# Optimization experiments

Hardware: AMD Instinct MI355X
Metric: run time of the kernel (lower is better)

## Reference

```python
import jax, jax.numpy as jnp
import numpy as np

N, DIM, H, D = 8192, 1152, 16, 72
SEGS = 4  # equal-length image segments


def setup_inputs() -> dict:
    key = jax.random.key(0)
    ks = jax.random.split(key, 8)
    s = 0.02
    return {
        "hidden_states": jax.random.normal(ks[0], (N, DIM), jnp.float32),
        "cos": jax.random.uniform(ks[1], (N, D), jnp.float32, -1.0, 1.0),
        "sin": jax.random.uniform(ks[2], (N, D), jnp.float32, -1.0, 1.0),
        "cu_seqlens": (jnp.arange(SEGS + 1, dtype=jnp.int32) * (N // SEGS)),
        "w_qkv": jax.random.normal(ks[3], (DIM, 3 * DIM), jnp.float32) * s,
        "b_qkv": jax.random.normal(ks[4], (3 * DIM,), jnp.float32) * s,
        "w_proj": jax.random.normal(ks[5], (DIM, DIM), jnp.float32) * s,
        "b_proj": jax.random.normal(ks[6], (DIM,), jnp.float32) * s,
    }


def _rope(x, cos, sin):
    # x: [N, H, D]; cos/sin: [N, 1, D]
    half = x.shape[-1] // 2
    x1, x2 = x[..., :half], x[..., half:]
    rot = jnp.concatenate([-x2, x1], axis=-1)
    return x * cos + rot * sin


def reference(hidden_states, cos, sin, cu_seqlens, w_qkv, b_qkv, w_proj, b_proj):
    n = hidden_states.shape[0]
    qkv = (hidden_states @ w_qkv + b_qkv).reshape(n, 3, H, D)
    q, k, v = qkv[:, 0], qkv[:, 1], qkv[:, 2]
    c = cos[:, None, :]
    s = sin[:, None, :]
    q = _rope(q, c, s)
    k = _rope(k, c, s)
    # equal-length segments derived statically from cu_seqlens
    segs = int(cu_seqlens.shape[0]) - 1
    L = n // segs
    qs = q.reshape(segs, L, H, D)
    ks = k.reshape(segs, L, H, D)
    vs = v.reshape(segs, L, H, D)
    scale = D ** -0.5
    scores = jnp.einsum("slhd,smhd->shlm", qs, ks) * scale
    attn = jax.nn.softmax(scores, axis=-1)
    out = jnp.einsum("shlm,smhd->slhd", attn, vs).reshape(n, DIM)
    return out @ w_proj + b_proj
```

## Files before the change

kernel.cpp:

```cpp
#include <hip/hip_runtime.h>
#include <hip/hip_bf16.h>
#include <cstdint>
#include <cstddef>

typedef __bf16 bf16;
typedef __attribute__((ext_vector_type(8))) __bf16 bf16x8;
typedef __attribute__((ext_vector_type(4))) float f32x4;
typedef __attribute__((ext_vector_type(16))) float f32x16;
typedef __attribute__((ext_vector_type(4))) float floatx4;
typedef __attribute__((ext_vector_type(4))) unsigned short ushort4_t;

#define NTOK 8192
#define DIMM 1152
#define NH   16
#define HD   72
#define SEGS 4
#define SEGL 2048

__device__ __forceinline__ void gload16(const void* gsrc, void* ldst) {
  __builtin_amdgcn_global_load_lds(
      (const __attribute__((address_space(1))) void*)gsrc,
      (__attribute__((address_space(3))) void*)ldst,
      16, 0, 0);
}

__device__ __forceinline__ unsigned pk2(float a, float b) {
  unsigned short x = __builtin_bit_cast(unsigned short, (bf16)a);
  unsigned short y = __builtin_bit_cast(unsigned short, (bf16)b);
  return (unsigned)x | ((unsigned)y << 16);
}

__global__ __launch_bounds__(256) void k_cvt(const float* __restrict__ src,
                                             bf16* __restrict__ dst, int n8) {
  int i = blockIdx.x * 256 + threadIdx.x;
  if (i >= n8) return;
  const floatx4* s = (const floatx4*)src + (size_t)i * 2;
  floatx4 a = s[0], b = s[1];
  bf16x8 o;
  o[0] = (bf16)a.x; o[1] = (bf16)a.y; o[2] = (bf16)a.z; o[3] = (bf16)a.w;
  o[4] = (bf16)b.x; o[5] = (bf16)b.y; o[6] = (bf16)b.z; o[7] = (bf16)b.w;
  *((bf16x8*)dst + i) = o;
}

__global__ __launch_bounds__(256) void k_twt(const float* __restrict__ src,
                                             bf16* __restrict__ dst, int R, int C) {
  __shared__ bf16 tile[64][73];
  int bc = blockIdx.x * 64, br = blockIdx.y * 64;
  int t = threadIdx.x;
#pragma unroll
  for (int i = 0; i < 16; i++) {
    int idx = i * 256 + t;
    int r = idx >> 6, c = idx & 63;
    float v = (bc + c < C) ? src[(size_t)(br + r) * C + bc + c] : 0.f;
    tile[c][r] = (bf16)v;
  }
  __syncthreads();
#pragma unroll
  for (int i = 0; i < 16; i++) {
    int idx = i * 256 + t;
    int r = idx >> 6, c = idx & 63;
    dst[(size_t)(bc + r) * R + br + c] = tile[r][c];
  }
}

template <int BM, int BN, int MI, int NI, int THREADS, bool OUT_F32>
__global__ __launch_bounds__(THREADS, 2) void k_gemmP(const bf16* __restrict__ A,
                                                      const bf16* __restrict__ Bt,
                                                      const float* __restrict__ bias,
                                                      void* __restrict__ Cout,
                                                      int M, int Nreal, int K, int gx) {
  __shared__ bf16 sA[2][BM * 32];
  __shared__ bf16 sB[2][BN * 32];
  constexpr int WN = BN / (NI * 16);
  constexpr int nA = (BM * 4) / THREADS;
  constexpr int nB = (BN * 4) / THREADS;
  constexpr int NLD = nA + nB;
  static_assert(NLD == 3 || NLD == 4, "vmcnt literal");
  const int t = threadIdx.x, wave = t >> 6, lane = t & 63;
  const int lr = lane & 15, lg = lane >> 4;
  const int nwg = gridDim.x, bid = blockIdx.x;
  const int swz = (bid & 7) * (nwg >> 3) + (bid >> 3);
  const int bx = swz % gx, by = swz / gx;
  const int m0 = by * BM, n0 = bx * BN;
  const int wr = wave / WN, wc = wave % WN;
  const int NS = K >> 5;

  f32x4 acc[MI][NI];
#pragma unroll
  for (int i = 0; i < MI; i++)
#pragma unroll
    for (int j = 0; j < NI; j++)
#pragma unroll
      for (int q = 0; q < 4; q++) acc[i][j][q] = 0.f;

  const bf16* Ab = A + (size_t)m0 * K;
  const bf16* Bb = Bt + (size_t)n0 * K;
  const int glsw = ((t & 3) ^ ((t >> 3) & 3)) * 8;
  const int rbase = t >> 2;

  auto STAGE = [&](int slot, int k0) {
#pragma unroll
    for (int p = 0; p < nA; ++p)
      gload16(Ab + (size_t)(rbase + p * (THREADS / 4)) * K + k0 + glsw,
              (char*)&sA[slot][0] + p * (THREADS * 16) + wave * 1024);
#pragma unroll
    for (int p = 0; p < nB; ++p)
      gload16(Bb + (size_t)(rbase + p * (THREADS / 4)) * K + k0 + glsw,
              (char*)&sB[slot][0] + p * (THREADS * 16) + wave * 1024);
  };

  const int swz4 = (lr >> 1) & 3;
  const int aoff = (wr * MI * 16 + lr) * 32 + ((lg ^ swz4) * 8);
  const int boff = (wc * NI * 16 + lr) * 32 + ((lg ^ swz4) * 8);

  STAGE(0, 0);
  STAGE(1, 32);

  for (int j = 0; j < NS; ++j) {
    const int slot = j & 1;
    if (j == NS - 1) {
      asm volatile("s_waitcnt vmcnt(0)" ::: "memory");
    } else if constexpr (NLD == 3) {
      asm volatile("s_waitcnt vmcnt(3)" ::: "memory");
    } else {
      asm volatile("s_waitcnt vmcnt(4)" ::: "memory");
    }
    __builtin_amdgcn_s_barrier();
    __builtin_amdgcn_sched_barrier(0);
    bf16x8 av[MI], bv[NI];
#pragma unroll
    for (int mi = 0; mi < MI; mi++)
      av[mi] = *(const bf16x8*)&sA[slot][aoff + mi * 512];
#pragma unroll
    for (int ni = 0; ni < NI; ni++)
      bv[ni] = *(const bf16x8*)&sB[slot][boff + ni * 512];
    asm volatile("s_waitcnt lgkmcnt(0)" ::: "memory");
    __builtin_amdgcn_sched_barrier(0);
    __builtin_amdgcn_s_barrier();
    if (j + 2 < NS) STAGE(slot, (j + 2) * 32);
    __builtin_amdgcn_s_setprio(1);
#pragma unroll
    for (int mi = 0; mi < MI; mi++)
#pragma unroll
      for (int ni = 0; ni < NI; ni++)
        acc[mi][ni] = __builtin_amdgcn_mfma_f32_16x16x32_bf16(av[mi], bv[ni], acc[mi][ni], 0, 0, 0);
    __builtin_amdgcn_s_setprio(0);
  }

#pragma unroll
  for (int mi = 0; mi < MI; ++mi)
#pragma unroll
    for (int ni = 0; ni < NI; ++ni) {
      int col = n0 + wc * NI * 16 + ni * 16 + lr;
      if (col < Nreal) {
        float bc_ = bias[col];
#pragma unroll
        for (int j = 0; j < 4; j++) {
          int row = m0 + wr * MI * 16 + mi * 16 + lg * 4 + j;
          float v = acc[mi][ni][j] + bc_;
          if (OUT_F32)
            ((float*)Cout)[(size_t)row * Nreal + col] = v;
          else
            ((bf16*)Cout)[(size_t)row * Nreal + col] = (bf16)v;
        }
      }
    }
}

__global__ __launch_bounds__(256) void k_rope(const bf16* __restrict__ qkv,
                                              const float* __restrict__ cs,
                                              const float* __restrict__ sn,
                                              bf16* __restrict__ Qp,
                                              bf16* __restrict__ Kp) {
  int n = blockIdx.x;
  int s = n >> 11, l = n & 2047;
  const bf16* row = qkv + (size_t)n * (3 * DIMM);
  const float* cr = cs + (size_t)n * HD;
  const float* sr = sn + (size_t)n * HD;
  const float QS = 0.17002323f;
  for (int e = threadIdx.x; e < 3072; e += 256) {
    int which = e / 1536;
    int r = e - which * 1536;
    int h = r / 96;
    int d = r - h * 96;
    float v = 0.f;
    if (d < HD) {
      int base = which * DIMM + h * HD;
      float x = (float)row[base + d];
      float o = (d < 36) ? -(float)row[base + d + 36] : (float)row[base + d - 36];
      v = x * cr[d] + o * sr[d];
      if (which == 0) v *= QS;
    }
    bf16* dst = which ? Kp : Qp;
    dst[(((size_t)(s * NH + h) * 3 + (d >> 5)) * SEGL + l) * 32 + (d & 31)] = (bf16)v;
  }
}

__global__ __launch_bounds__(256) void k_vrep(const bf16* __restrict__ qkv,
                                              bf16* __restrict__ Vt) {
  int s = blockIdx.z, h = blockIdx.y, l0 = blockIdx.x * 64;
  __shared__ bf16 tl[64][73];
  int t = threadIdx.x;
  for (int idx = t; idx < 64 * HD; idx += 256) {
    int l = idx / HD, d = idx - l * HD;
    tl[l][d] = qkv[(size_t)(s * SEGL + l0 + l) * (3 * DIMM) + 2 * DIMM + h * HD + d];
  }
  __syncthreads();
  for (int idx = t; idx < 96 * 64; idx += 256) {
    int d = idx >> 6, l = idx & 63;
    bf16 v = (d < HD) ? tl[l][d] : ((d == HD) ? (bf16)1.f : (bf16)0.f);
    Vt[((size_t)(s * NH + h) * 96 + d) * SEGL + l0 + l] = v;
  }
}

__global__ __launch_bounds__(256, 2) void k_attn(const bf16* __restrict__ Qg,
                                                 const bf16* __restrict__ Kg,
                                                 const bf16* __restrict__ Vg,
                                                 bf16* __restrict__ Oo) {
  __shared__ bf16 sK[2][3 * 64 * 32];
  __shared__ bf16 sV[2][96 * 64];
  const int t = threadIdx.x, wave = t >> 6, lane = t & 63;
  const int c = lane & 31, hi = lane >> 5;
  const int s = blockIdx.z, h = blockIdx.y, q0 = blockIdx.x * 256;
  const bf16* Qb = Qg + (size_t)(s * NH + h) * 3 * SEGL * 32;
  const bf16* Kb = Kg + (size_t)(s * NH + h) * 3 * SEGL * 32;
  const bf16* Vb = Vg + (size_t)(s * NH + h) * 96 * SEGL;

  auto STAGEKV = [&](int kv0, int b) {
#pragma unroll
    for (int i = 0; i < 3; i++) {
      int ch = wave * 3 + i;
      int kk = ch >> 2;
      int r = (ch & 3) * 16 + (lane >> 2);
      int g = (lane & 3) ^ ((r >> 1) & 3);
      gload16(Kb + (size_t)kk * (SEGL * 32) + (size_t)(kv0 + r) * 32 + g * 8,
              (char*)sK[b] + ch * 1024);
    }
#pragma unroll
    for (int i = 0; i < 3; i++) {
      int ch = wave * 3 + i;
      int r = ch * 8 + (lane >> 3);
      int g = (lane & 7) ^ (r & 7);
      gload16(Vb + (size_t)r * SEGL + kv0 + g * 8, (char*)sV[b] + ch * 1024);
    }
  };

  bf16x8 Qf[2][5];
#pragma unroll
  for (int sni = 0; sni < 2; sni++)
#pragma unroll
    for (int kk = 0; kk < 5; kk++) {
      int qr = q0 + wave * 64 + sni * 32 + c;
      Qf[sni][kk] = *(const bf16x8*)&Qb[(size_t)(kk >> 1) * (SEGL * 32) +
                                        (size_t)qr * 32 + ((kk & 1) * 2 + hi) * 8];
    }

  f32x16 accO[3][2];
#pragma unroll
  for (int df = 0; df < 3; df++)
#pragma unroll
    for (int sni = 0; sni < 2; sni++)
#pragma unroll
      for (int r = 0; r < 16; r++) accO[df][sni][r] = 0.f;

  f32x16 S[2][2];

  auto QKT = [&](int b) {
#pragma unroll
    for (int smi = 0; smi < 2; smi++)
#pragma unroll
      for (int sni = 0; sni < 2; sni++)
#pragma unroll
        for (int r = 0; r < 16; r++) S[smi][sni][r] = 0.f;
    __builtin_amdgcn_s_setprio(1);
#pragma unroll
    for (int kk = 0; kk < 5; kk++) {
      bf16x8 Kf[2];
#pragma unroll
      for (int smi = 0; smi < 2; smi++) {
        int kr = smi * 32 + c;
        int g = (((kk & 1) * 2 + hi) ^ ((kr >> 1) & 3));
        Kf[smi] = *(const bf16x8*)&sK[b][(kk >> 1) * 2048 + kr * 32 + g * 8];
      }
#pragma unroll
      for (int smi = 0; smi < 2; smi++)
#pragma unroll
        for (int sni = 0; sni < 2; sni++)
          S[smi][sni] = __builtin_amdgcn_mfma_f32_32x32x16_bf16(Kf[smi], Qf[sni][kk], S[smi][sni], 0, 0, 0);
    }
    __builtin_amdgcn_s_setprio(0);
  };

  STAGEKV(0, 0);
  STAGEKV(64, 1);
  __syncthreads();
  QKT(0);

  for (int tile = 0; tile < 32; ++tile) {
    const int buf = tile & 1;
#pragma unroll
    for (int half = 0; half < 2; ++half) {
      unsigned pbu[2][2][4];
#pragma unroll
      for (int k2 = 0; k2 < 2; ++k2)
#pragma unroll
        for (int sni = 0; sni < 2; sni++) {
          const int base = k2 * 8;
          unsigned u0 = pk2(__builtin_amdgcn_exp2f(S[half][sni][base + 0]),
                            __builtin_amdgcn_exp2f(S[half][sni][base + 1]));
          unsigned u1 = pk2(__builtin_amdgcn_exp2f(S[half][sni][base + 2]),
                            __builtin_amdgcn_exp2f(S[half][sni][base + 3]));
          unsigned u2 = pk2(__builtin_amdgcn_exp2f(S[half][sni][base + 4]),
                            __builtin_amdgcn_exp2f(S[half][sni][base + 5]));
          unsigned u3 = pk2(__builtin_amdgcn_exp2f(S[half][sni][base + 6]),
                            __builtin_amdgcn_exp2f(S[half][sni][base + 7]));
          asm volatile("v_permlane32_swap_b32 %0, %1" : "+v"(u0), "+v"(u2));
          asm volatile("v_permlane32_swap_b32 %0, %1" : "+v"(u1), "+v"(u3));
          pbu[k2][sni][0] = u0; pbu[k2][sni][1] = u1;
          pbu[k2][sni][2] = u2; pbu[k2][sni][3] = u3;
        }
      __builtin_amdgcn_s_setprio(1);
#pragma unroll
      for (int k2 = 0; k2 < 2; ++k2) {
        const int kk = half * 2 + k2;
        bf16x8 Vf[3];
#pragma unroll
        for (int df = 0; df < 3; df++) {
          int dr = df * 32 + c;
          int g = ((kk * 2 + hi) ^ (dr & 7));
          Vf[df] = *(const bf16x8*)&sV[buf][dr * 64 + g * 8];
        }
#pragma unroll
        for (int sni = 0; sni < 2; sni++) {
          union { bf16x8 v; unsigned u[4]; } pb;
          pb.u[0] = pbu[k2][sni][0]; pb.u[1] = pbu[k2][sni][1];
          pb.u[2] = pbu[k2][sni][2]; pb.u[3] = pbu[k2][sni][3];
#pragma unroll
          for (int df = 0; df < 3; df++)
            accO[df][sni] = __builtin_amdgcn_mfma_f32_32x32x16_bf16(Vf[df], pb.v, accO[df][sni], 0, 0, 0);
        }
      }
      __builtin_amdgcn_s_setprio(0);
    }

    if (tile + 1 < 32) {
      __syncthreads();
      if (tile + 2 < 32) STAGEKV((tile + 2) * 64, buf);
      QKT(buf ^ 1);
    }
  }

#pragma unroll
  for (int sni = 0; sni < 2; sni++) {
    float lown = accO[2][sni][4];
    float lv = lown + __shfl_xor(lown, 32, 64);
    float inv = 1.f / lv;
    int token = s * SEGL + q0 + wave * 64 + sni * 32 + c;
#pragma unroll
    for (int df = 0; df < 3; df++)
#pragma unroll
      for (int rg = 0; rg < 4; rg++) {
        int d0 = df * 32 + rg * 8 + hi * 4;
        if (d0 < HD) {
          ushort4_t w;
          w[0] = __builtin_bit_cast(unsigned short, (bf16)(accO[df][sni][rg * 4 + 0] * inv));
          w[1] = __builtin_bit_cast(unsigned short, (bf16)(accO[df][sni][rg * 4 + 1] * inv));
          w[2] = __builtin_bit_cast(unsigned short, (bf16)(accO[df][sni][rg * 4 + 2] * inv));
          w[3] = __builtin_bit_cast(unsigned short, (bf16)(accO[df][sni][rg * 4 + 3] * inv));
          *(ushort4_t*)&Oo[(size_t)token * DIMM + h * HD + d0] = w;
        }
      }
  }
}

extern "C" void kernel_launch(void* const* d_in, const int* in_sizes, int n_in,
                              void* d_out, int out_size, void* d_ws, size_t ws_size,
                              hipStream_t stream) {
  (void)in_sizes; (void)n_in; (void)out_size; (void)ws_size;
  const float* hs     = (const float*)d_in[0];
  const float* cosp   = (const float*)d_in[1];
  const float* sinp   = (const float*)d_in[2];
  const float* w_qkv  = (const float*)d_in[4];
  const float* b_qkv  = (const float*)d_in[5];
  const float* w_proj = (const float*)d_in[6];
  const float* b_proj = (const float*)d_in[7];
  float* out = (float*)d_out;

  char* ws = (char*)d_ws;
  bf16* hsb    = (bf16*)(ws + 0);
  bf16* wprojT = (bf16*)(ws + 26836992);
  bf16* qkv    = (bf16*)(ws + 29491200);
  bf16* Qp     = (bf16*)(ws + 86114304);
  bf16* Kp     = (bf16*)(ws + 111280128);
  bf16* Vt     = (bf16*)(ws + 136445952);
  bf16* ao     = (bf16*)(ws + 161611776);
  bf16* wqkvT  = (bf16*)(ws + 161611776);

  k_cvt<<<4608, 256, 0, stream>>>(hs, hsb, 1179648);
  k_twt<<<dim3(56, 18), 256, 0, stream>>>(w_qkv, wqkvT, 1152, 3456);
  k_twt<<<dim3(18, 18), 256, 0, stream>>>(w_proj, wprojT, 1152, 1152);
  k_gemmP<128, 256, 4, 4, 512, false><<<896, 512, 0, stream>>>(
      hsb, wqkvT, b_qkv, (void*)qkv, 8192, 3456, 1152, 14);
  k_rope<<<8192, 256, 0, stream>>>(qkv, cosp, sinp, Qp, Kp);
  k_vrep<<<dim3(32, 16, 4), 256, 0, stream>>>(qkv, Vt);
  k_attn<<<dim3(8, 16, 4), 256, 0, stream>>>(Qp, Kp, Vt, ao);
  k_gemmP<128, 128, 4, 4, 256, true><<<576, 256, 0, stream>>>(
      ao, wprojT, b_proj, (void*)out, 8192, 1152, 1152, 9);
}
```

Before: 301.1 us.

## Triple-buffer GEMM LDS stages and restructure attention loop with swizzled block mapping

```diff
diff --git a/kernel.cpp b/kernel.cpp
--- a/kernel.cpp
+++ b/kernel.cpp
@@ -69,8 +69,8 @@
                                                       const float* __restrict__ bias,
                                                       void* __restrict__ Cout,
                                                       int M, int Nreal, int K, int gx) {
-  __shared__ bf16 sA[2][BM * 32];
-  __shared__ bf16 sB[2][BN * 32];
+  __shared__ bf16 sA[3][BM * 32];
+  __shared__ bf16 sB[3][BN * 32];
   constexpr int WN = BN / (NI * 16);
   constexpr int nA = (BM * 4) / THREADS;
   constexpr int nB = (BN * 4) / THREADS;
@@ -116,8 +116,8 @@
   STAGE(0, 0);
   STAGE(1, 32);
 
+  int slot = 0;
   for (int j = 0; j < NS; ++j) {
-    const int slot = j & 1;
     if (j == NS - 1) {
       asm volatile("s_waitcnt vmcnt(0)" ::: "memory");
     } else if constexpr (NLD == 3) {
@@ -136,8 +136,10 @@
       bv[ni] = *(const bf16x8*)&sB[slot][boff + ni * 512];
     asm volatile("s_waitcnt lgkmcnt(0)" ::: "memory");
     __builtin_amdgcn_sched_barrier(0);
-    __builtin_amdgcn_s_barrier();
-    if (j + 2 < NS) STAGE(slot, (j + 2) * 32);
+    if (j + 2 < NS) {
+      int s2 = slot + 2; if (s2 >= 3) s2 -= 3;
+      STAGE(s2, (j + 2) * 32);
+    }
     __builtin_amdgcn_s_setprio(1);
 #pragma unroll
     for (int mi = 0; mi < MI; mi++)
@@ -145,6 +147,7 @@
       for (int ni = 0; ni < NI; ni++)
         acc[mi][ni] = __builtin_amdgcn_mfma_f32_16x16x32_bf16(av[mi], bv[ni], acc[mi][ni], 0, 0, 0);
     __builtin_amdgcn_s_setprio(0);
+    if (++slot == 3) slot = 0;
   }
 
 #pragma unroll
@@ -221,29 +224,13 @@
   __shared__ bf16 sV[2][96 * 64];
   const int t = threadIdx.x, wave = t >> 6, lane = t & 63;
   const int c = lane & 31, hi = lane >> 5;
-  const int s = blockIdx.z, h = blockIdx.y, q0 = blockIdx.x * 256;
+  const int bid = blockIdx.x;
+  const int g = ((bid >> 6) << 3) | (bid & 7);
+  const int qt = (bid >> 3) & 7;
+  const int s = g >> 4, h = g & 15, q0 = qt * 256;
   const bf16* Qb = Qg + (size_t)(s * NH + h) * 3 * SEGL * 32;
   const bf16* Kb = Kg + (size_t)(s * NH + h) * 3 * SEGL * 32;
   const bf16* Vb = Vg + (size_t)(s * NH + h) * 96 * SEGL;
-
-  auto STAGEKV = [&](int kv0, int b) {
-#pragma unroll
-    for (int i = 0; i < 3; i++) {
-      int ch = wave * 3 + i;
-      int kk = ch >> 2;
-      int r = (ch & 3) * 16 + (lane >> 2);
-      int g = (lane & 3) ^ ((r >> 1) & 3);
-      gload16(Kb + (size_t)kk * (SEGL * 32) + (size_t)(kv0 + r) * 32 + g * 8,
-              (char*)sK[b] + ch * 1024);
-    }
-#pragma unroll
-    for (int i = 0; i < 3; i++) {
-      int ch = wave * 3 + i;
-      int r = ch * 8 + (lane >> 3);
-      int g = (lane & 7) ^ (r & 7);
-      gload16(Vb + (size_t)r * SEGL + kv0 + g * 8, (char*)sV[b] + ch * 1024);
-    }
-  };
 
   bf16x8 Qf[2][5];
 #pragma unroll
@@ -255,6 +242,24 @@
                                         (size_t)qr * 32 + ((kk & 1) * 2 + hi) * 8];
     }
 
+#pragma unroll
+  for (int i = 0; i < 3; i++) {
+    int ch = wave * 3 + i;
+    int kk = ch >> 2;
+    int r = (ch & 3) * 16 + (lane >> 2);
+    int gg = (lane & 3) ^ ((r >> 1) & 3);
+    gload16(Kb + (size_t)kk * (SEGL * 32) + (size_t)r * 32 + gg * 8,
+            (char*)sK[0] + ch * 1024);
+  }
+#pragma unroll
+  for (int i = 0; i < 3; i++) {
+    int ch = wave * 3 + i;
+    int r = ch * 8 + (lane >> 3);
+    int gg = (lane & 7) ^ (r & 7);
+    gload16(Vb + (size_t)r * SEGL + gg * 8, (char*)sV[0] + ch * 1024);
+  }
+  __syncthreads();
+
   f32x16 accO[3][2];
 #pragma unroll
   for (int df = 0; df < 3; df++)
@@ -262,16 +267,33 @@
     for (int sni = 0; sni < 2; sni++)
 #pragma unroll
       for (int r = 0; r < 16; r++) accO[df][sni][r] = 0.f;
-
-  f32x16 S[2][2];
-
-  auto QKT = [&](int b) {
-#pragma unroll
-    for (int smi = 0; smi < 2; smi++)
-#pragma unroll
-      for (int sni = 0; sni < 2; sni++)
-#pragma unroll
-        for (int r = 0; r < 16; r++) S[smi][sni][r] = 0.f;
+  f32x16 ZC;
+#pragma unroll
+  for (int r = 0; r < 16; r++) ZC[r] = 0.f;
+
+  int cur = 0;
+  for (int tile = 0; tile < 32; ++tile) {
+    if (tile + 1 < 32) {
+      int kv0 = (tile + 1) * 64;
+#pragma unroll
+      for (int i = 0; i < 3; i++) {
+        int ch = wave * 3 + i;
+        int kk = ch >> 2;
+        int r = (ch & 3) * 16 + (lane >> 2);
+        int gg = (lane & 3) ^ ((r >> 1) & 3);
+        gload16(Kb + (size_t)kk * (SEGL * 32) + (size_t)(kv0 + r) * 32 + gg * 8,
+                (char*)sK[cur ^ 1] + ch * 1024);
+      }
+#pragma unroll
+      for (int i = 0; i < 3; i++) {
+        int ch = wave * 3 + i;
+        int r = ch * 8 + (lane >> 3);
+        int gg = (lane & 7) ^ (r & 7);
+        gload16(Vb + (size_t)r * SEGL + kv0 + gg * 8, (char*)sV[cur ^ 1] + ch * 1024);
+      }
+    }
+
+    f32x16 S[2][2];
     __builtin_amdgcn_s_setprio(1);
 #pragma unroll
     for (int kk = 0; kk < 5; kk++) {
@@ -279,75 +301,53 @@
 #pragma unroll
       for (int smi = 0; smi < 2; smi++) {
         int kr = smi * 32 + c;
-        int g = (((kk & 1) * 2 + hi) ^ ((kr >> 1) & 3));
-        Kf[smi] = *(const bf16x8*)&sK[b][(kk >> 1) * 2048 + kr * 32 + g * 8];
+        int gg = (((kk & 1) * 2 + hi) ^ ((kr >> 1) & 3));
+        Kf[smi] = *(const bf16x8*)&sK[cur][(kk >> 1) * 2048 + kr * 32 + gg * 8];
       }
 #pragma unroll
       for (int smi = 0; smi < 2; smi++)
 #pragma unroll
         for (int sni = 0; sni < 2; sni++)
-          S[smi][sni] = __builtin_amdgcn_mfma_f32_32x32x16_bf16(Kf[smi], Qf[sni][kk], S[smi][sni], 0, 0, 0);
+          S[smi][sni] = __builtin_amdgcn_mfma_f32_32x32x16_bf16(
+              Kf[smi], Qf[sni][kk], kk ? S[smi][sni] : ZC, 0, 0, 0);
     }
     __builtin_amdgcn_s_setprio(0);
-  };
-
-  STAGEKV(0, 0);
-  STAGEKV(64, 1);
-  __syncthreads();
-  QKT(0);
-
-  for (int tile = 0; tile < 32; ++tile) {
-    const int buf = tile & 1;
-#pragma unroll
-    for (int half = 0; half < 2; ++half) {
-      unsigned pbu[2][2][4];
-#pragma unroll
-      for (int k2 = 0; k2 < 2; ++k2)
-#pragma unroll
-        for (int sni = 0; sni < 2; sni++) {
-          const int base = k2 * 8;
-          unsigned u0 = pk2(__builtin_amdgcn_exp2f(S[half][sni][base + 0]),
-                            __builtin_amdgcn_exp2f(S[half][sni][base + 1]));
-          unsigned u1 = pk2(__builtin_amdgcn_exp2f(S[half][sni][base + 2]),
-                            __builtin_amdgcn_exp2f(S[half][sni][base + 3]));
-          unsigned u2 = pk2(__builtin_amdgcn_exp2f(S[half][sni][base + 4]),
-                            __builtin_amdgcn_exp2f(S[half][sni][base + 5]));
-          unsigned u3 = pk2(__builtin_amdgcn_exp2f(S[half][sni][base + 6]),
-                            __builtin_amdgcn_exp2f(S[half][sni][base + 7]));
-          asm volatile("v_permlane32_swap_b32 %0, %1" : "+v"(u0), "+v"(u2));
-          asm volatile("v_permlane32_swap_b32 %0, %1" : "+v"(u1), "+v"(u3));
-          pbu[k2][sni][0] = u0; pbu[k2][sni][1] = u1;
-          pbu[k2][sni][2] = u2; pbu[k2][sni][3] = u3;
-        }
-      __builtin_amdgcn_s_setprio(1);
-#pragma unroll
-      for (int k2 = 0; k2 < 2; ++k2) {
-        const int kk = half * 2 + k2;
-        bf16x8 Vf[3];
-#pragma unroll
-        for (int df = 0; df < 3; df++) {
-          int dr = df * 32 + c;
-          int g = ((kk * 2 + hi) ^ (dr & 7));
-          Vf[df] = *(const bf16x8*)&sV[buf][dr * 64 + g * 8];
-        }
-#pragma unroll
-        for (int sni = 0; sni < 2; sni++) {
-          union { bf16x8 v; unsigned u[4]; } pb;
-          pb.u[0] = pbu[k2][sni][0]; pb.u[1] = pbu[k2][sni][1];
-          pb.u[2] = pbu[k2][sni][2]; pb.u[3] = pbu[k2][sni][3];
-#pragma unroll
-          for (int df = 0; df < 3; df++)
-            accO[df][sni] = __builtin_amdgcn_mfma_f32_32x32x16_bf16(Vf[df], pb.v, accO[df][sni], 0, 0, 0);
-        }
-      }
-      __builtin_amdgcn_s_setprio(0);
-    }
-
-    if (tile + 1 < 32) {
-      __syncthreads();
-      if (tile + 2 < 32) STAGEKV((tile + 2) * 64, buf);
-      QKT(buf ^ 1);
-    }
+
+    __builtin_amdgcn_s_setprio(1);
+#pragma unroll
+    for (int kk = 0; kk < 4; kk++) {
+      bf16x8 Vf[3];
+#pragma unroll
+      for (int df = 0; df < 3; df++) {
+        int dr = df * 32 + c;
+        int gg = ((kk * 2 + hi) ^ (dr & 7));
+        Vf[df] = *(const bf16x8*)&sV[cur][dr * 64 + gg * 8];
+      }
+#pragma unroll
+      for (int sni = 0; sni < 2; sni++) {
+        const int smi = kk >> 1;
+        const int base = (kk & 1) * 8;
+        unsigned u0 = pk2(__builtin_amdgcn_exp2f(S[smi][sni][base + 0]),
+                          __builtin_amdgcn_exp2f(S[smi][sni][base + 1]));
+        unsigned u1 = pk2(__builtin_amdgcn_exp2f(S[smi][sni][base + 2]),
+                          __builtin_amdgcn_exp2f(S[smi][sni][base + 3]));
+        unsigned u2 = pk2(__builtin_amdgcn_exp2f(S[smi][sni][base + 4]),
+                          __builtin_amdgcn_exp2f(S[smi][sni][base + 5]));
+        unsigned u3 = pk2(__builtin_amdgcn_exp2f(S[smi][sni][base + 6]),
+                          __builtin_amdgcn_exp2f(S[smi][sni][base + 7]));
+        asm volatile("v_permlane32_swap_b32 %0, %1" : "+v"(u0), "+v"(u2));
+        asm volatile("v_permlane32_swap_b32 %0, %1" : "+v"(u1), "+v"(u3));
+        union { bf16x8 v; unsigned u[4]; } pb;
+        pb.u[0] = u0; pb.u[1] = u1; pb.u[2] = u2; pb.u[3] = u3;
+#pragma unroll
+        for (int df = 0; df < 3; df++)
+          accO[df][sni] = __builtin_amdgcn_mfma_f32_32x32x16_bf16(Vf[df], pb.v, accO[df][sni], 0, 0, 0);
+      }
+    }
+    __builtin_amdgcn_s_setprio(0);
+
+    __syncthreads();
+    cur ^= 1;
   }
 
 #pragma unroll
@@ -403,7 +403,7 @@
       hsb, wqkvT, b_qkv, (void*)qkv, 8192, 3456, 1152, 14);
   k_rope<<<8192, 256, 0, stream>>>(qkv, cosp, sinp, Qp, Kp);
   k_vrep<<<dim3(32, 16, 4), 256, 0, stream>>>(qkv, Vt);
-  k_attn<<<dim3(8, 16, 4), 256, 0, stream>>>(Qp, Kp, Vt, ao);
+  k_attn<<<512, 256, 0, stream>>>(Qp, Kp, Vt, ao);
   k_gemmP<128, 128, 4, 4, 256, true><<<576, 256, 0, stream>>>(
       ao, wprojT, b_proj, (void*)out, 8192, 1152, 1152, 9);
 }
```

After: 293.9 us. -2.4%, faster.
